# Performance work log

Measured on AMD Instinct MI355X. Metric: run time of the kernel, lower is better.

The kernel has to match this reference:

```python
import jax, jax.numpy as jnp
import numpy as np

B, XL, YL, D = 16, 2048, 2048, 1024

def setup_inputs() -> dict:
    key = jax.random.key(0)
    kx, ky, km, kw = jax.random.split(key, 4)
    x = jax.random.normal(kx, (B, XL, D), dtype=jnp.float32)
    y = jax.random.normal(ky, (B, YL, D), dtype=jnp.float32)
    # True == padding position (masked with -inf in the torch module)
    y_mask = jax.random.randint(km, (B, YL), 0, 2).astype(bool)
    # shared projection Linear(embed_dim, embed_dim); scale ~ 1/sqrt(D)
    W = jax.random.normal(kw, (D, D), dtype=jnp.float32) * (1.0 / np.sqrt(D))
    b = jnp.zeros((D,), dtype=jnp.float32)
    return {"x": x, "y": y, "y_mask": y_mask, "W": W, "b": b}

def reference(x, y, y_mask, W, b):
    # shared ReLU(Linear) projection applied to both x and y
    x_proj = jax.nn.relu(jnp.einsum('bxd,ed->bxe', x, W) + b)   # (B, XL, D)
    y_proj = jax.nn.relu(jnp.einsum('byd,ed->bye', y, W) + b)   # (B, YL, D)
    scores = jnp.einsum('bxd,byd->bxy', x_proj, y_proj)          # (B, XL, YL)
    scores = jnp.where(y_mask[:, None, :], -jnp.inf, scores)
    weights = jax.nn.softmax(scores, axis=2)
    contexts = jnp.einsum('bxy,byd->bxd', weights, y)            # (B, XL, D)
    return contexts
```

## Files before the change

kernel.cpp:

```cpp
#include <hip/hip_runtime.h>
#include <math.h>
#include <stdint.h>


typedef __attribute__((ext_vector_type(8))) _Float16 f16x8;
typedef __attribute__((ext_vector_type(4))) float f32x4;

__device__ __forceinline__ ushort h2u(_Float16 h) { return __builtin_bit_cast(ushort, h); }

__device__ __forceinline__ void ld16(const ushort* g, ushort* l) {
    __builtin_amdgcn_global_load_lds(
        (__attribute__((address_space(1))) void*)(g),
        (__attribute__((address_space(3))) void*)(l), 16, 0, 0);
}

#define BAR()  { __builtin_amdgcn_s_barrier(); asm volatile("" ::: "memory"); }
#define VMW(N) asm volatile("s_waitcnt vmcnt(" #N ")" ::: "memory");
#define LG(N)  { asm volatile("s_waitcnt lgkmcnt(" #N ")" ::: "memory"); __builtin_amdgcn_sched_barrier(0); }

template<int EPI, int MODE>
__global__ __launch_bounds__(512) void gemm256(
    const ushort* __restrict__ A, size_t zsA,
    const ushort* __restrict__ B, size_t zsB,
    const float* __restrict__ bias, const int* __restrict__ nyBuf,
    float* __restrict__ Cf, ushort* __restrict__ Chi, size_t zsC,
    int sdA, int sdB, int N, int T)
{
    __shared__ char ldsb[131072];

    const int gx = gridDim.x, gxy = gx * gridDim.y;
    const int total = gxy * gridDim.z;
    int hsw = blockIdx.z * gxy + blockIdx.y * gx + blockIdx.x;
    hsw = (hsw & 7) * (total >> 3) + (hsw >> 3);
    const int z = hsw / gxy;
    const int rem = hsw - z * gxy;
    const int by = rem / gx;
    const int bx = rem - by * gx;

    int NY = 0, NYPAD = 0;
    if constexpr (MODE != 0) { NY = nyBuf[2 * z]; NYPAD = nyBuf[2 * z + 1]; }
    if constexpr (MODE == 1) { if (by * 256 >= 2048 && by * 256 - 2048 >= NYPAD) return; }
    if constexpr (MODE == 2) { if (bx * 256 >= NYPAD) return; }
    if constexpr (MODE == 3) { T = NYPAD >> 6; }

    const int tid = threadIdx.x;
    const int lane = tid & 63;
    const int wv = tid >> 6, wm = wv >> 2, wn = wv & 3;
    const int m0 = by * 256, n0 = bx * 256;

    const int pl  = tid >> 3;
    const int ss  = (tid & 7) ^ (pl & 7);
    const int sr0 = 2 * pl + (ss >> 2);
    const int ske = (ss & 3) * 8;
    const int tb  = tid * 16;

    const ushort* gA0 = A + (size_t)z * zsA + (size_t)(m0 + sr0) * sdA + ske;
    const ushort* gA1 = A + (size_t)z * zsA + (size_t)(m0 + 128 + sr0) * sdA + ske;
    const ushort* gB0 = B + (size_t)z * zsB + (size_t)(n0 + sr0) * sdB + ske;
    const ushort* gB1 = B + (size_t)z * zsB + (size_t)(n0 + 128 + sr0) * sdB + ske;

#define ST_A(KOF, DOF) { ld16(gA0 + (KOF), (ushort*)(ldsb + (DOF) + tb));          \
                         ld16(gA1 + (KOF), (ushort*)(ldsb + (DOF) + 8192 + tb)); }
#define ST_B(KOF, DOF) { ld16(gB0 + (KOF), (ushort*)(ldsb + 65536 + (DOF) + tb));  \
                         ld16(gB1 + (KOF), (ushort*)(ldsb + 65536 + (DOF) + 8192 + tb)); }

    const int fr = lane & 15, fq = lane >> 4;
    const int sl = (((fr & 1) << 2) | fq) ^ ((fr >> 1) & 7);
    const int aoff = (wm * 64 + (fr >> 1)) * 128 + sl * 16;
    const int boff = (wn * 32 + (fr >> 1)) * 128 + sl * 16;

    f32x4 acc[8][4];
    #pragma unroll
    for (int i = 0; i < 8; ++i)
        #pragma unroll
        for (int j = 0; j < 4; ++j)
            acc[i][j] = (f32x4){0.f, 0.f, 0.f, 0.f};

    f16x8 a0[4], a1[4], bb0[4], bb1[4];

#define RD4(DST, BASE) { const char* p_ = (BASE);                                  \
    DST[0] = *(const f16x8*)(p_);        DST[1] = *(const f16x8*)(p_ + 1024);      \
    DST[2] = *(const f16x8*)(p_ + 2048); DST[3] = *(const f16x8*)(p_ + 3072); }
#define MFL(AV, BV) { __builtin_amdgcn_s_setprio(1);                               \
    _Pragma("unroll") for (int m_ = 0; m_ < 4; ++m_)                               \
        _Pragma("unroll") for (int n_ = 0; n_ < 4; ++n_)                           \
            acc[m_][n_] = __builtin_amdgcn_mfma_f32_16x16x32_f16(AV[m_], BV[n_], acc[m_][n_], 0, 0, 0); \
    __builtin_amdgcn_s_setprio(0); }
#define MFH(AV, BV) { __builtin_amdgcn_s_setprio(1);                               \
    _Pragma("unroll") for (int m_ = 0; m_ < 4; ++m_)                               \
        _Pragma("unroll") for (int n_ = 0; n_ < 4; ++n_)                           \
            acc[m_ + 4][n_] = __builtin_amdgcn_mfma_f32_16x16x32_f16(AV[m_], BV[n_], acc[m_ + 4][n_], 0, 0, 0); \
    __builtin_amdgcn_s_setprio(0); }

#define TILE(D0, D1, DN, S0, S1, S2, S3, V0, V2)                                   \
    RD4(a1, ldsb + (D0) + aoff + 4096);                                            \
    S0; BAR(); LG(4); MFL(a0, bb0); V0; BAR();                                     \
    RD4(bb1, ldsb + 65536 + (D1) + boff); RD4(a0, ldsb + (D1) + aoff);             \
    S1; BAR(); LG(8); MFH(a1, bb0); BAR();                                         \
    RD4(a1, ldsb + (D1) + aoff + 4096);                                            \
    S2; BAR(); LG(4); MFL(a0, bb1); V2; BAR();                                     \
    RD4(bb0, ldsb + 65536 + (DN) + boff); RD4(a0, ldsb + (DN) + aoff);             \
    S3; BAR(); LG(8); MFH(a1, bb1); BAR();

    ST_A(0, 0);      ST_B(0, 0);
    ST_A(32, 16384); ST_B(32, 16384);
    ST_A(64, 32768); ST_B(64, 32768);
    VMW(8);
    BAR();
    RD4(bb0, ldsb + 65536 + boff);
    RD4(a0, ldsb + aoff);

    for (int it = 0; it < (T - 2) / 2; ++it) {
        TILE(0, 16384, 32768,
             ST_A(96, 49152), ST_B(96, 49152), ST_A(128, 0), ST_B(128, 0),
             VMW(6), VMW(6))
        TILE(32768, 49152, 0,
             ST_A(160, 16384), ST_B(160, 16384), ST_A(192, 32768), ST_B(192, 32768),
             VMW(6), VMW(6))
        gA0 += 128; gA1 += 128; gB0 += 128; gB1 += 128;
    }
    TILE(0, 16384, 32768, ST_A(96, 49152), ST_B(96, 49152), , , VMW(6), VMW(4))
    TILE(32768, 49152, 32768, , , , , VMW(0), )

    #pragma unroll
    for (int n = 0; n < 4; ++n) {
        const int col = n0 + wn * 64 + n * 16 + fr;
        float bb = 0.f;
        if constexpr (EPI == 1) bb = bias[col];
        #pragma unroll
        for (int m = 0; m < 8; ++m) {
            const int row = m0 + wm * 128 + m * 16 + fq * 4;
            #pragma unroll
            for (int r = 0; r < 4; ++r) {
                const float v = acc[m][n][r];
                const size_t idx = (size_t)z * zsC + (size_t)(row + r) * N + col;
                if constexpr (EPI == 0) {
                    Cf[idx] = v;
                } else if constexpr (EPI == 1) {
                    Chi[idx] = h2u((_Float16)fmaxf(v + bb, 0.f));
                } else {
                    Cf[idx] = (col >= NY) ? -INFINITY : v;
                }
            }
        }
    }
#undef ST_A
#undef ST_B
#undef RD4
#undef MFL
#undef MFH
#undef TILE
}

__global__ __launch_bounds__(256) void build_idx(const int* __restrict__ mask,
    int* __restrict__ idx, int* __restrict__ nyBuf)
{
    const int z = blockIdx.x;
    const int* mb = mask + (size_t)z * 2048;
    __shared__ int part[256];
    const int tid = threadIdx.x;
    int keep[8]; int c = 0;
    #pragma unroll
    for (int k = 0; k < 8; ++k) { keep[k] = (mb[tid * 8 + k] == 0); c += keep[k]; }
    part[tid] = c;
    for (int off = 1; off < 256; off <<= 1) {
        __syncthreads();
        const int v = (tid >= off) ? part[tid - off] : 0;
        __syncthreads();
        part[tid] += v;
    }
    __syncthreads();
    int pos = part[tid] - c;
    #pragma unroll
    for (int k = 0; k < 8; ++k)
        if (keep[k]) idx[(size_t)z * 2048 + (pos++)] = tid * 8 + k;
    if (tid == 255) {
        const int ny = part[255];
        int nyp = (ny + 127) & ~127;
        if (nyp < 256) nyp = 256;
        nyBuf[2 * z] = ny;
        nyBuf[2 * z + 1] = nyp;
    }
}

__global__ __launch_bounds__(256) void cvt_f16(const float* __restrict__ in,
    ushort* __restrict__ o, size_t sIn4, size_t sOut)
{
    const size_t z = blockIdx.z;
    const int i = blockIdx.x * 256 + threadIdx.x;
    const float4 v = reinterpret_cast<const float4*>(in)[z * sIn4 + i];
    ushort4 h;
    h.x = h2u((_Float16)v.x); h.y = h2u((_Float16)v.y);
    h.z = h2u((_Float16)v.z); h.w = h2u((_Float16)v.w);
    reinterpret_cast<ushort4*>(o + z * sOut)[i] = h;
}

__global__ __launch_bounds__(256) void gather_y(const float* __restrict__ y,
    const int* __restrict__ idx, const int* __restrict__ nyBuf,
    ushort* __restrict__ rH, ushort* __restrict__ tT,
    size_t sIn, size_t sR, size_t sT)
{
    __shared__ float tile[32][33];
    const size_t z = blockIdx.z;
    const int NY = nyBuf[2 * z], NYPAD = nyBuf[2 * z + 1];
    const int r0 = blockIdx.y * 32;
    if (r0 >= NYPAD) return;
    const int c0 = blockIdx.x * 32;
    const float* yb = y + z * sIn;
    const int* idxb = idx + z * 2048;
    const int tx = threadIdx.x & 31, ty = threadIdx.x >> 5;
    #pragma unroll
    for (int k = 0; k < 4; ++k) {
        const int i = r0 + ty + k * 8;
        float v = 0.f;
        if (i < NY) v = yb[(size_t)idxb[i] * 1024 + c0 + tx];
        tile[ty + k * 8][tx] = v;
        rH[z * sR + (size_t)i * 1024 + c0 + tx] = h2u((_Float16)v);
    }
    __syncthreads();
    #pragma unroll
    for (int k = 0; k < 4; ++k) {
        const int c = c0 + ty + k * 8;
        tT[z * sT + (size_t)c * 2048 + r0 + tx] = h2u((_Float16)tile[tx][ty + k * 8]);
    }
}

__global__ __launch_bounds__(256) void softmax_f16(const float* __restrict__ S,
    ushort* __restrict__ Wout, const int* __restrict__ nyBuf, size_t sS, size_t sW)
{
    const size_t row = blockIdx.x;
    const size_t b = row >> 11, r = row & 2047;
    const int nf4 = nyBuf[2 * b + 1] >> 2;
    const float4* p4 = reinterpret_cast<const float4*>(S + b * sS + r * 2048);
    ushort4* q4 = reinterpret_cast<ushort4*>(Wout + b * sW + r * 2048);
    const int tid = threadIdx.x;

    const float4 NEG = {-INFINITY, -INFINITY, -INFINITY, -INFINITY};
    float4 v0 = (tid < nf4) ? p4[tid] : NEG;
    float4 v1 = (tid + 256 < nf4) ? p4[tid + 256] : NEG;
    float m = fmaxf(fmaxf(fmaxf(v0.x, v0.y), fmaxf(v0.z, v0.w)),
                    fmaxf(fmaxf(v1.x, v1.y), fmaxf(v1.z, v1.w)));
    #pragma unroll
    for (int off = 32; off >= 1; off >>= 1)
        m = fmaxf(m, __shfl_xor(m, off));

    __shared__ float redm[4], reds[4];
    if ((tid & 63) == 0) redm[tid >> 6] = m;
    __syncthreads();
    m = fmaxf(fmaxf(redm[0], redm[1]), fmaxf(redm[2], redm[3]));

    float e[8];
    e[0] = __expf(v0.x - m); e[1] = __expf(v0.y - m);
    e[2] = __expf(v0.z - m); e[3] = __expf(v0.w - m);
    e[4] = __expf(v1.x - m); e[5] = __expf(v1.y - m);
    e[6] = __expf(v1.z - m); e[7] = __expf(v1.w - m);
    float s = ((e[0] + e[1]) + (e[2] + e[3])) + ((e[4] + e[5]) + (e[6] + e[7]));
    #pragma unroll
    for (int off = 32; off >= 1; off >>= 1)
        s += __shfl_xor(s, off);
    if ((tid & 63) == 0) reds[tid >> 6] = s;
    __syncthreads();
    s = reds[0] + reds[1] + reds[2] + reds[3];

    const float inv = 1.f / s;
    ushort4 o0, o1;
    o0.x = h2u((_Float16)(e[0] * inv)); o0.y = h2u((_Float16)(e[1] * inv));
    o0.z = h2u((_Float16)(e[2] * inv)); o0.w = h2u((_Float16)(e[3] * inv));
    o1.x = h2u((_Float16)(e[4] * inv)); o1.y = h2u((_Float16)(e[5] * inv));
    o1.z = h2u((_Float16)(e[6] * inv)); o1.w = h2u((_Float16)(e[7] * inv));
    if (tid < nf4) q4[tid] = o0;
    if (tid + 256 < nf4) q4[tid + 256] = o1;
}

extern "C" void kernel_launch(void* const* d_in, const int* in_sizes, int n_in,
                              void* d_out, int out_size, void* d_ws, size_t ws_size,
                              hipStream_t stream)
{
    const float* x    = (const float*)d_in[0];
    const float* y    = (const float*)d_in[1];
    const int* ymask  = (const int*)d_in[2];
    const float* W    = (const float*)d_in[3];
    const float* bias = (const float*)d_in[4];
    float* out = (float*)d_out;

    const size_t BD = 2097152;

    const size_t perBatch = 29360128ull;
    int G = 16;
    while (G > 1 && 4194304ull + (size_t)G * perBatch > ws_size) G >>= 1;

    uint8_t* wsb = (uint8_t*)d_ws;
    ushort* W16  = (ushort*)wsb;
    int* idxBuf  = (int*)(wsb + 2097152);
    int* nyBuf   = (int*)(wsb + 2097152 + 131072);
    uint8_t* r1  = wsb + 4194304;
    uint8_t* r2  = r1 + (size_t)G * 16777216;
    uint8_t* r3  = r2 + (size_t)G * 8388608;

    ushort* xyHi = (ushort*)r1;
    float*  sc   = (float*)r1;
    ushort* pHi  = (ushort*)r2;
    ushort* yT   = (ushort*)r3;

    cvt_f16<<<dim3(1024, 1, 1), dim3(256), 0, stream>>>(W, W16, 0, 0);
    build_idx<<<dim3(16), dim3(256), 0, stream>>>(ymask, idxBuf, nyBuf);

    for (int bs = 0; bs < 16; bs += G) {
        const float* xg = x + (size_t)bs * BD;
        const float* yg = y + (size_t)bs * BD;
        const int* nyB  = nyBuf + 2 * bs;

        cvt_f16<<<dim3(2048, 1, G), dim3(256), 0, stream>>>(
            xg, xyHi, BD / 4, 8388608);
        gather_y<<<dim3(32, 64, G), dim3(256), 0, stream>>>(
            yg, idxBuf + (size_t)bs * 2048, nyB,
            xyHi + BD, yT, BD, 8388608, BD);

        gemm256<1, 1><<<dim3(4, 16, G), dim3(512), 0, stream>>>(
            xyHi, 8388608, W16, 0,
            bias, nyB,
            nullptr, pHi, 4194304, 1024, 1024, 1024, 16);

        gemm256<2, 2><<<dim3(8, 8, G), dim3(512), 0, stream>>>(
            pHi, 4194304, pHi + BD, 4194304,
            nullptr, nyB,
            sc, nullptr, 4194304, 1024, 1024, 2048, 16);

        softmax_f16<<<dim3(G * 2048), dim3(256), 0, stream>>>(
            sc, pHi, nyB, 4194304, 4194304);

        gemm256<0, 3><<<dim3(4, 8, G), dim3(512), 0, stream>>>(
            pHi, 4194304, yT, 2097152,
            nullptr, nyB,
            out + (size_t)bs * BD, nullptr, BD, 2048, 2048, 1024, 32);
    }
}
```

Measured before the change: 503.4 us.

## Replace 256x256 pipelined GEMM with simpler 128x128 double-buffered GEMM

```diff
diff --git a/kernel.cpp b/kernel.cpp
--- a/kernel.cpp
+++ b/kernel.cpp
@@ -14,19 +14,15 @@
         (__attribute__((address_space(3))) void*)(l), 16, 0, 0);
 }
 
-#define BAR()  { __builtin_amdgcn_s_barrier(); asm volatile("" ::: "memory"); }
-#define VMW(N) asm volatile("s_waitcnt vmcnt(" #N ")" ::: "memory");
-#define LG(N)  { asm volatile("s_waitcnt lgkmcnt(" #N ")" ::: "memory"); __builtin_amdgcn_sched_barrier(0); }
-
 template<int EPI, int MODE>
-__global__ __launch_bounds__(512) void gemm256(
+__global__ __launch_bounds__(256) void gemm128(
     const ushort* __restrict__ A, size_t zsA,
     const ushort* __restrict__ B, size_t zsB,
     const float* __restrict__ bias, const int* __restrict__ nyBuf,
     float* __restrict__ Cf, ushort* __restrict__ Chi, size_t zsC,
     int sdA, int sdB, int N, int T)
 {
-    __shared__ char ldsb[131072];
+    __shared__ char ldsb[32768];
 
     const int gx = gridDim.x, gxy = gx * gridDim.y;
     const int total = gxy * gridDim.z;
@@ -39,14 +35,15 @@
 
     int NY = 0, NYPAD = 0;
     if constexpr (MODE != 0) { NY = nyBuf[2 * z]; NYPAD = nyBuf[2 * z + 1]; }
-    if constexpr (MODE == 1) { if (by * 256 >= 2048 && by * 256 - 2048 >= NYPAD) return; }
-    if constexpr (MODE == 2) { if (bx * 256 >= NYPAD) return; }
-    if constexpr (MODE == 3) { T = NYPAD >> 6; }
+    if constexpr (MODE == 1) { if (by * 128 >= 2048 && by * 128 - 2048 >= NYPAD) return; }
+    if constexpr (MODE == 2) { if (bx * 128 >= NYPAD) return; }
+    if constexpr (MODE == 3) { T = NYPAD >> 5; }
 
     const int tid = threadIdx.x;
     const int lane = tid & 63;
-    const int wv = tid >> 6, wm = wv >> 2, wn = wv & 3;
-    const int m0 = by * 256, n0 = bx * 256;
+    const int wv = tid >> 6;
+    const int wm = (wv >> 1) * 64, wn = (wv & 1) * 64;
+    const int m0 = by * 128, n0 = bx * 128;
 
     const int pl  = tid >> 3;
     const int ss  = (tid & 7) ^ (pl & 7);
@@ -55,84 +52,66 @@
     const int tb  = tid * 16;
 
     const ushort* gA0 = A + (size_t)z * zsA + (size_t)(m0 + sr0) * sdA + ske;
-    const ushort* gA1 = A + (size_t)z * zsA + (size_t)(m0 + 128 + sr0) * sdA + ske;
+    const ushort* gA1 = gA0 + (size_t)64 * sdA;
     const ushort* gB0 = B + (size_t)z * zsB + (size_t)(n0 + sr0) * sdB + ske;
-    const ushort* gB1 = B + (size_t)z * zsB + (size_t)(n0 + 128 + sr0) * sdB + ske;
-
-#define ST_A(KOF, DOF) { ld16(gA0 + (KOF), (ushort*)(ldsb + (DOF) + tb));          \
-                         ld16(gA1 + (KOF), (ushort*)(ldsb + (DOF) + 8192 + tb)); }
-#define ST_B(KOF, DOF) { ld16(gB0 + (KOF), (ushort*)(ldsb + 65536 + (DOF) + tb));  \
-                         ld16(gB1 + (KOF), (ushort*)(ldsb + 65536 + (DOF) + 8192 + tb)); }
+    const ushort* gB1 = gB0 + (size_t)64 * sdB;
 
     const int fr = lane & 15, fq = lane >> 4;
     const int sl = (((fr & 1) << 2) | fq) ^ ((fr >> 1) & 7);
-    const int aoff = (wm * 64 + (fr >> 1)) * 128 + sl * 16;
-    const int boff = (wn * 32 + (fr >> 1)) * 128 + sl * 16;
-
-    f32x4 acc[8][4];
-    #pragma unroll
-    for (int i = 0; i < 8; ++i)
+    const int aoff = wm * 64 + (fr >> 1) * 128 + sl * 16;
+    const int boff = 8192 + wn * 64 + (fr >> 1) * 128 + sl * 16;
+
+    f32x4 acc[4][4];
+    #pragma unroll
+    for (int i = 0; i < 4; ++i)
         #pragma unroll
         for (int j = 0; j < 4; ++j)
             acc[i][j] = (f32x4){0.f, 0.f, 0.f, 0.f};
 
-    f16x8 a0[4], a1[4], bb0[4], bb1[4];
-
-#define RD4(DST, BASE) { const char* p_ = (BASE);                                  \
-    DST[0] = *(const f16x8*)(p_);        DST[1] = *(const f16x8*)(p_ + 1024);      \
-    DST[2] = *(const f16x8*)(p_ + 2048); DST[3] = *(const f16x8*)(p_ + 3072); }
-#define MFL(AV, BV) { __builtin_amdgcn_s_setprio(1);                               \
-    _Pragma("unroll") for (int m_ = 0; m_ < 4; ++m_)                               \
-        _Pragma("unroll") for (int n_ = 0; n_ < 4; ++n_)                           \
-            acc[m_][n_] = __builtin_amdgcn_mfma_f32_16x16x32_f16(AV[m_], BV[n_], acc[m_][n_], 0, 0, 0); \
-    __builtin_amdgcn_s_setprio(0); }
-#define MFH(AV, BV) { __builtin_amdgcn_s_setprio(1);                               \
-    _Pragma("unroll") for (int m_ = 0; m_ < 4; ++m_)                               \
-        _Pragma("unroll") for (int n_ = 0; n_ < 4; ++n_)                           \
-            acc[m_ + 4][n_] = __builtin_amdgcn_mfma_f32_16x16x32_f16(AV[m_], BV[n_], acc[m_ + 4][n_], 0, 0, 0); \
-    __builtin_amdgcn_s_setprio(0); }
-
-#define TILE(D0, D1, DN, S0, S1, S2, S3, V0, V2)                                   \
-    RD4(a1, ldsb + (D0) + aoff + 4096);                                            \
-    S0; BAR(); LG(4); MFL(a0, bb0); V0; BAR();                                     \
-    RD4(bb1, ldsb + 65536 + (D1) + boff); RD4(a0, ldsb + (D1) + aoff);             \
-    S1; BAR(); LG(8); MFH(a1, bb0); BAR();                                         \
-    RD4(a1, ldsb + (D1) + aoff + 4096);                                            \
-    S2; BAR(); LG(4); MFL(a0, bb1); V2; BAR();                                     \
-    RD4(bb0, ldsb + 65536 + (DN) + boff); RD4(a0, ldsb + (DN) + aoff);             \
-    S3; BAR(); LG(8); MFH(a1, bb1); BAR();
-
-    ST_A(0, 0);      ST_B(0, 0);
-    ST_A(32, 16384); ST_B(32, 16384);
-    ST_A(64, 32768); ST_B(64, 32768);
-    VMW(8);
-    BAR();
-    RD4(bb0, ldsb + 65536 + boff);
-    RD4(a0, ldsb + aoff);
-
-    for (int it = 0; it < (T - 2) / 2; ++it) {
-        TILE(0, 16384, 32768,
-             ST_A(96, 49152), ST_B(96, 49152), ST_A(128, 0), ST_B(128, 0),
-             VMW(6), VMW(6))
-        TILE(32768, 49152, 0,
-             ST_A(160, 16384), ST_B(160, 16384), ST_A(192, 32768), ST_B(192, 32768),
-             VMW(6), VMW(6))
-        gA0 += 128; gA1 += 128; gB0 += 128; gB1 += 128;
-    }
-    TILE(0, 16384, 32768, ST_A(96, 49152), ST_B(96, 49152), , , VMW(6), VMW(4))
-    TILE(32768, 49152, 32768, , , , , VMW(0), )
-
-    #pragma unroll
-    for (int n = 0; n < 4; ++n) {
-        const int col = n0 + wn * 64 + n * 16 + fr;
+    auto stage = [&](int buf) {
+        char* d = ldsb + buf * 16384;
+        ld16(gA0, (ushort*)(d + tb));
+        ld16(gA1, (ushort*)(d + 4096 + tb));
+        ld16(gB0, (ushort*)(d + 8192 + tb));
+        ld16(gB1, (ushort*)(d + 12288 + tb));
+        gA0 += 32; gA1 += 32; gB0 += 32; gB1 += 32;
+    };
+    auto compute = [&](int buf) {
+        const char* p = ldsb + buf * 16384;
+        f16x8 a[4], b[4];
+        #pragma unroll
+        for (int i = 0; i < 4; ++i) a[i] = *(const f16x8*)(p + aoff + i * 1024);
+        #pragma unroll
+        for (int j = 0; j < 4; ++j) b[j] = *(const f16x8*)(p + boff + j * 1024);
+        #pragma unroll
+        for (int i = 0; i < 4; ++i)
+            #pragma unroll
+            for (int j = 0; j < 4; ++j)
+                acc[i][j] = __builtin_amdgcn_mfma_f32_16x16x32_f16(a[i], b[j], acc[i][j], 0, 0, 0);
+    };
+
+    stage(0);
+    __syncthreads();
+    int cur = 0;
+    for (int t = 0; t < T - 1; ++t) {
+        stage(cur ^ 1);
+        compute(cur);
+        __syncthreads();
+        cur ^= 1;
+    }
+    compute(cur);
+
+    #pragma unroll
+    for (int j = 0; j < 4; ++j) {
+        const int col = n0 + wn + j * 16 + fr;
         float bb = 0.f;
         if constexpr (EPI == 1) bb = bias[col];
         #pragma unroll
-        for (int m = 0; m < 8; ++m) {
-            const int row = m0 + wm * 128 + m * 16 + fq * 4;
+        for (int i = 0; i < 4; ++i) {
+            const int row = m0 + wm + i * 16 + fq * 4;
             #pragma unroll
             for (int r = 0; r < 4; ++r) {
-                const float v = acc[m][n][r];
+                const float v = acc[i][j][r];
                 const size_t idx = (size_t)z * zsC + (size_t)(row + r) * N + col;
                 if constexpr (EPI == 0) {
                     Cf[idx] = v;
@@ -144,12 +123,6 @@
             }
         }
     }
-#undef ST_A
-#undef ST_B
-#undef RD4
-#undef MFL
-#undef MFH
-#undef TILE
 }
 
 __global__ __launch_bounds__(256) void build_idx(const int* __restrict__ mask,
@@ -316,20 +289,20 @@
             yg, idxBuf + (size_t)bs * 2048, nyB,
             xyHi + BD, yT, BD, 8388608, BD);
 
-        gemm256<1, 1><<<dim3(4, 16, G), dim3(512), 0, stream>>>(
+        gemm128<1, 1><<<dim3(8, 32, G), dim3(256), 0, stream>>>(
             xyHi, 8388608, W16, 0,
             bias, nyB,
-            nullptr, pHi, 4194304, 1024, 1024, 1024, 16);
-
-        gemm256<2, 2><<<dim3(8, 8, G), dim3(512), 0, stream>>>(
+            nullptr, pHi, 4194304, 1024, 1024, 1024, 32);
+
+        gemm128<2, 2><<<dim3(16, 16, G), dim3(256), 0, stream>>>(
             pHi, 4194304, pHi + BD, 4194304,
             nullptr, nyB,
-            sc, nullptr, 4194304, 1024, 1024, 2048, 16);
+            sc, nullptr, 4194304, 1024, 1024, 2048, 32);
 
         softmax_f16<<<dim3(G * 2048), dim3(256), 0, stream>>>(
             sc, pHi, nyB, 4194304, 4194304);
 
-        gemm256<0, 3><<<dim3(4, 8, G), dim3(512), 0, stream>>>(
+        gemm128<0, 3><<<dim3(8, 16, G), dim3(256), 0, stream>>>(
             pHi, 4194304, yT, 2097152,
             nullptr, nyB,
             out + (size_t)bs * BD, nullptr, BD, 2048, 2048, 1024, 32);
```

After: 510.4 us. Within noise of the previous version (+1.4%).
